# Kernel optimization log

Measured on AMD Instinct MI355X. Metric: run time of the kernel, lower is better.

The kernel has to match this reference:

```python
import jax, jax.numpy as jnp
import numpy as np

N, E, H, C = 50000, 800000, 4, 32   # nodes, edges, heads, per-head channels
EMB = 64                              # embedding_dim
VOCAB = 1000                          # input_dim (label vocab)


def _gat_layer(x, src, dst, W, a_src, a_dst, b):
    """PyG GATConv (concat heads, negative_slope=0.2, self-loops already in src/dst)."""
    n = x.shape[0]
    h = (x @ W).reshape(n, H, -1)                 # [N,H,C]
    al_s = (h * a_src).sum(-1)                    # [N,H]
    al_d = (h * a_dst).sum(-1)                    # [N,H]
    e = jax.nn.leaky_relu(al_s[src] + al_d[dst], 0.2)   # [E',H]
    m = jax.ops.segment_max(e, dst, num_segments=n)     # segment softmax (stable)
    p = jnp.exp(e - m[dst])
    s = jax.ops.segment_sum(p, dst, num_segments=n)
    alpha = p / (s[dst] + 1e-16)                  # [E',H]
    out = jax.ops.segment_sum(h[src] * alpha[..., None], dst, num_segments=n)
    return out.reshape(n, -1) + b                 # [N,H*C]


def setup_inputs() -> dict:
    key = jax.random.key(0)
    ks = jax.random.split(key, 16)
    def w(k, shape):
        return jax.random.normal(k, shape, jnp.float32) * 0.1
    return dict(
        label=jax.random.randint(ks[0], (N,), 0, VOCAB),
        edge_index=jax.random.randint(ks[1], (2, E), 0, N),
        weight=jax.random.uniform(ks[2], (E,), jnp.float32),
        request_quantity=jax.random.uniform(ks[3], (N,), jnp.float32),
        emb_table=w(ks[4], (VOCAB, EMB)),
        req_W=w(ks[5], (1, EMB)),
        req_b=jnp.zeros((EMB,), jnp.float32),
        W0=w(ks[6], (2 * EMB, H * C)), a_src0=w(ks[7], (H, C)), a_dst0=w(ks[8], (H, C)), b0=jnp.zeros((H * C,), jnp.float32),
        W1=w(ks[9], (H * C, H * C)), a_src1=w(ks[10], (H, C)), a_dst1=w(ks[11], (H, C)), b1=jnp.zeros((H * C,), jnp.float32),
        W2=w(ks[12], (H * C, H * C)), a_src2=w(ks[13], (H, C)), a_dst2=w(ks[14], (H, C)), b2=jnp.zeros((H * C,), jnp.float32),
    )


def reference(label, edge_index, weight, request_quantity, emb_table, req_W, req_b,
              W0, a_src0, a_dst0, b0, W1, a_src1, a_dst1, b1, W2, a_src2, a_dst2, b2):
    del weight  # GATConv(edge_dim=None): edge weights are not used in attention
    x_emb = emb_table[label]                                  # [N,EMB]
    rq = request_quantity
    rq = (rq - rq.mean()) / (rq.std(ddof=1) + 1e-6)           # torch std uses ddof=1
    req = rq[:, None] @ req_W + req_b                         # [N,EMB]
    x = jnp.concatenate([x_emb, req], axis=-1)                # [N,2*EMB]
    # PyG GATConv adds self-loops by default
    loops = jnp.arange(N)
    src = jnp.concatenate([edge_index[0], loops])
    dst = jnp.concatenate([edge_index[1], loops])
    gelu = lambda t: jax.nn.gelu(t, approximate=False)        # torch nn.GELU is exact
    x = gelu(_gat_layer(x, src, dst, W0, a_src0, a_dst0, b0))
    x = gelu(_gat_layer(x, src, dst, W1, a_src1, a_dst1, b1))
    x = gelu(_gat_layer(x, src, dst, W2, a_src2, a_dst2, b2))
    return x
```

## Files before the change

### kernel.cpp

```cpp
#include <hip/hip_runtime.h>
#include <hip/hip_fp16.h>
#include <math.h>

#define NN 50000
#define NE 800000
#define HC 128
#define NHEAD 4
#define EMB 64
#define STATS_BLOCKS 64
#define NB 196
#define HIST_BLOCKS 196
#define WPREP_BLOCKS 192
#define WT_ROW 136

typedef _Float16 f16x8 __attribute__((ext_vector_type(8)));
typedef float f32x4 __attribute__((ext_vector_type(4)));

__device__ __forceinline__ float lrelu(float x) { return x > 0.0f ? x : 0.2f * x; }
__device__ __forceinline__ float gelu_f(float x) {
    return 0.5f * x * (1.0f + erff(x * 0.70710678118654752440f));
}
__device__ __forceinline__ float sel4(float4 v, int h) {
    float r = v.x;
    r = (h == 1) ? v.y : r;
    r = (h == 2) ? v.z : r;
    r = (h == 3) ? v.w : r;
    return r;
}
__device__ __forceinline__ f16x8 cvt8(float4 a, float4 b) {
    f16x8 v;
    v[0] = (_Float16)a.x; v[1] = (_Float16)a.y; v[2] = (_Float16)a.z; v[3] = (_Float16)a.w;
    v[4] = (_Float16)b.x; v[5] = (_Float16)b.y; v[6] = (_Float16)b.z; v[7] = (_Float16)b.w;
    return v;
}

__global__ void prep_kernel(const float* __restrict__ rq, float* __restrict__ stats,
                            const int* __restrict__ dst, int* __restrict__ bucketCnt,
                            const float* __restrict__ W0, const float* __restrict__ W1,
                            const float* __restrict__ W2, _Float16* __restrict__ wt) {
    __shared__ float ls[4], ls2[4];
    __shared__ int cnt[NB];
    if (blockIdx.x < STATS_BLOCKS) {
        int i = blockIdx.x * 256 + threadIdx.x;
        float s = 0.f, s2 = 0.f;
        for (; i < NN; i += STATS_BLOCKS * 256) {
            float v = rq[i];
            s += v; s2 += v * v;
        }
        #pragma unroll
        for (int off = 32; off > 0; off >>= 1) {
            s  += __shfl_down(s, off);
            s2 += __shfl_down(s2, off);
        }
        int lane = threadIdx.x & 63, wid = threadIdx.x >> 6;
        if (lane == 0) { ls[wid] = s; ls2[wid] = s2; }
        __syncthreads();
        if (threadIdx.x == 0) {
            atomicAdd(&stats[0], ls[0] + ls[1] + ls[2] + ls[3]);
            atomicAdd(&stats[1], ls2[0] + ls2[1] + ls2[2] + ls2[3]);
        }
    } else if (blockIdx.x < STATS_BLOCKS + HIST_BLOCKS) {
        int bb = blockIdx.x - STATS_BLOCKS;
        for (int i = threadIdx.x; i < NB; i += 256) cnt[i] = 0;
        __syncthreads();
        int base = bb * 4096;
        #pragma unroll
        for (int it = 0; it < 16; it++) {
            int i = base + it * 256 + threadIdx.x;
            if (i < NE) atomicAdd(&cnt[dst[i] >> 8], 1);
        }
        __syncthreads();
        for (int i = threadIdx.x; i < NB; i += 256)
            if (cnt[i]) atomicAdd(&bucketCnt[i], cnt[i]);
    } else {
        int bb = blockIdx.x - STATS_BLOCKS - HIST_BLOCKS;
        int l = bb >> 6, blk = bb & 63;
        const float* W = (l == 0) ? W0 : (l == 1) ? W1 : W2;
        int idx = blk * 256 + threadIdx.x;
        int n = idx >> 7, k = idx & 127;
        wt[(size_t)l * 128 * WT_ROW + n * WT_ROW + k] = (_Float16)W[k * 128 + n];
    }
}

__device__ __forceinline__ void scan_buckets(const int* __restrict__ bucketCnt,
                                             int* sIncl ) {
    int t = threadIdx.x;
    int v = (t < NB) ? bucketCnt[t] : 0;
    sIncl[t] = v;
    __syncthreads();
    #pragma unroll
    for (int off = 1; off < 256; off <<= 1) {
        int add = (t >= off) ? sIncl[t - off] : 0;
        __syncthreads();
        sIncl[t] += add;
        __syncthreads();
    }
}

__global__ void binA_kernel(const int* __restrict__ src, const int* __restrict__ dst,
                            const int* __restrict__ bucketCnt, int* __restrict__ gcur,
                            int2* __restrict__ edge_tmp) {
    __shared__ int sIncl[256];
    __shared__ int sBaseE[256];
    __shared__ int cnt[NB];
    __shared__ int cur[NB];
    int t = threadIdx.x;
    scan_buckets(bucketCnt, sIncl);
    {
        int v = (t < NB) ? bucketCnt[t] : 0;
        sBaseE[t] = sIncl[t] - v;
    }
    for (int i = t; i < NB; i += 256) cnt[i] = 0;
    __syncthreads();
    int base = blockIdx.x * 4096;
    int d[16], s[16];
    #pragma unroll
    for (int it = 0; it < 16; it++) {
        int i = base + it * 256 + t;
        bool ok = i < NE;
        d[it] = ok ? dst[i] : -1;
        s[it] = ok ? src[i] : 0;
        if (ok) atomicAdd(&cnt[d[it] >> 8], 1);
    }
    __syncthreads();
    for (int i = t; i < NB; i += 256)
        cur[i] = cnt[i] ? (sBaseE[i] + atomicAdd(&gcur[i], cnt[i])) : 0;
    __syncthreads();
    #pragma unroll
    for (int it = 0; it < 16; it++) {
        if (d[it] >= 0) {
            int b = d[it] >> 8;
            int pos = atomicAdd(&cur[b], 1);
            edge_tmp[pos] = make_int2(s[it], d[it] & 255);
        }
    }
}

__global__ void binB_kernel(const int2* __restrict__ edge_tmp, const int* __restrict__ bucketCnt,
                            int* __restrict__ row_start, int* __restrict__ src_sorted) {
    __shared__ int sIncl[256];
    __shared__ int ldeg[256];
    __shared__ int lexcl[256];
    __shared__ int lcur[256];
    __shared__ int s_base, s_end;
    int b = blockIdx.x, t = threadIdx.x;
    scan_buckets(bucketCnt, sIncl);
    if (t == 0) {
        s_end = sIncl[b];
        s_base = sIncl[b] - bucketCnt[b];
    }
    ldeg[t] = 0;
    __syncthreads();
    int base = s_base, endb = s_end;
    for (int i = base + t; i < endb; i += 256)
        atomicAdd(&ldeg[edge_tmp[i].y], 1);
    __syncthreads();
    int v = ldeg[t];
    lexcl[t] = v;
    __syncthreads();
    #pragma unroll
    for (int off = 1; off < 256; off <<= 1) {
        int add = (t >= off) ? lexcl[t - off] : 0;
        __syncthreads();
        lexcl[t] += add;
        __syncthreads();
    }
    int excl = lexcl[t] - v;
    int node = b * 256 + t;
    if (node <= NN) row_start[node] = base + excl;
    lcur[t] = excl;
    __syncthreads();
    for (int i = base + t; i < endb; i += 256) {
        int2 e = edge_tmp[i];
        int pos = atomicAdd(&lcur[e.y], 1);
        src_sorted[base + pos] = e.x;
    }
}

template <int L0>
__launch_bounds__(256)
__global__ void gemm_al_kernel(const __half* __restrict__ xh, const _Float16* __restrict__ wt,
                               const float* __restrict__ a_src, const float* __restrict__ a_dst,
                               __half* __restrict__ h, float* __restrict__ als,
                               float* __restrict__ ald,
                               const int* __restrict__ label, const float* __restrict__ rq,
                               const float* __restrict__ emb, const float* __restrict__ reqW,
                               const float* __restrict__ reqb, const float* __restrict__ stats) {
    extern __shared__ char smem[];
    _Float16* sWt = (_Float16*)smem;
    _Float16* sX  = sWt + 128 * WT_ROW;
    int t = threadIdx.x;
    int w = t >> 6, l = t & 63;
    int col = l & 15, quad = l >> 4;
    int row0 = blockIdx.x * 64;

    {
        const f16x8* g = (const f16x8*)wt;
        f16x8* s = (f16x8*)sWt;
        #pragma unroll
        for (int i = 0; i < 9; i++) {
            int idx = t + 256 * i;
            if (idx < 128 * WT_ROW / 8) s[idx] = g[idx];
        }
    }
    if (L0) {
        float sum = stats[0], sumsq = stats[1];
        float mean = sum / (float)NN;
        float var = (sumsq - sum * sum / (float)NN) / (float)(NN - 1);
        float inv = 1.0f / (sqrtf(var) + 1e-6f);
        #pragma unroll
        for (int i = 0; i < 4; i++) {
            int idx = t + 256 * i;
            int r = idx >> 4;
            int q = idx & 15;
            int rr = row0 + r;
            f16x8 v;
            #pragma unroll
            for (int j = 0; j < 8; j++) v[j] = (_Float16)0.f;
            if (rr < NN) {
                if (q < 8) {
                    const float4* er = (const float4*)(emb + (size_t)label[rr] * EMB);
                    v = cvt8(er[q * 2], er[q * 2 + 1]);
                } else {
                    int j4 = (q - 8) * 2;
                    float4 w0 = ((const float4*)reqW)[j4],     b0 = ((const float4*)reqb)[j4];
                    float4 w1 = ((const float4*)reqW)[j4 + 1], b1 = ((const float4*)reqb)[j4 + 1];
                    float r2 = (rq[rr] - mean) * inv;
                    v = cvt8(make_float4(r2 * w0.x + b0.x, r2 * w0.y + b0.y,
                                         r2 * w0.z + b0.z, r2 * w0.w + b0.w),
                             make_float4(r2 * w1.x + b1.x, r2 * w1.y + b1.y,
                                         r2 * w1.z + b1.z, r2 * w1.w + b1.w));
                }
            }
            *(f16x8*)&sX[r * WT_ROW + q * 8] = v;
        }
    }
    __syncthreads();

    f16x8 afr[4];
    if (L0) {
        #pragma unroll
        for (int ks = 0; ks < 4; ks++)
            afr[ks] = *(const f16x8*)&sX[(w * 16 + col) * WT_ROW + ks * 32 + quad * 8];
    } else {
        int rr = row0 + w * 16 + col;
        const __half* xp = xh + (size_t)rr * 128;
        #pragma unroll
        for (int ks = 0; ks < 4; ks++)
            afr[ks] = *(const f16x8*)(xp + ks * 32 + quad * 8);
    }

    f32x4 zero = {0.f, 0.f, 0.f, 0.f};
    f32x4 acc[8];
    #pragma unroll
    for (int nt = 0; nt < 8; nt++) acc[nt] = zero;
    #pragma unroll
    for (int nt = 0; nt < 8; nt++) {
        #pragma unroll
        for (int ks = 0; ks < 4; ks++) {
            f16x8 bfr = *(const f16x8*)&sWt[(nt * 16 + col) * WT_ROW + ks * 32 + quad * 8];
            acc[nt] = __builtin_amdgcn_mfma_f32_16x16x32_f16(afr[ks], bfr, acc[nt], 0, 0, 0);
        }
    }
    __syncthreads();

    _Float16* sOut = sWt;
    #pragma unroll
    for (int nt = 0; nt < 8; nt++)
        #pragma unroll
        for (int r = 0; r < 4; r++)
            sOut[(w * 16 + quad * 4 + r) * WT_ROW + nt * 16 + col] = (_Float16)acc[nt][r];
    __builtin_amdgcn_wave_barrier();
    #pragma unroll
    for (int i = 0; i < 4; i++) {
        int u = l + 64 * i;
        int r = u >> 4, off = (u & 15) * 8;
        int rr = row0 + w * 16 + r;
        f16x8 v = *(const f16x8*)&sOut[(w * 16 + r) * WT_ROW + off];
        if (rr < NN) *(f16x8*)(h + (size_t)rr * 128 + off) = v;
    }

    float as[8], ad[8];
    #pragma unroll
    for (int nt = 0; nt < 8; nt++) {
        as[nt] = a_src[nt * 16 + col];
        ad[nt] = a_dst[nt * 16 + col];
    }
    #pragma unroll
    for (int r = 0; r < 4; r++) {
        float ps[4], pd[4];
        #pragma unroll
        for (int hd = 0; hd < 4; hd++) {
            ps[hd] = acc[2 * hd][r] * as[2 * hd] + acc[2 * hd + 1][r] * as[2 * hd + 1];
            pd[hd] = acc[2 * hd][r] * ad[2 * hd] + acc[2 * hd + 1][r] * ad[2 * hd + 1];
            ps[hd] += __shfl_xor(ps[hd], 1); pd[hd] += __shfl_xor(pd[hd], 1);
            ps[hd] += __shfl_xor(ps[hd], 2); pd[hd] += __shfl_xor(pd[hd], 2);
            ps[hd] += __shfl_xor(ps[hd], 4); pd[hd] += __shfl_xor(pd[hd], 4);
            ps[hd] += __shfl_xor(ps[hd], 8); pd[hd] += __shfl_xor(pd[hd], 8);
        }
        int rr = row0 + w * 16 + quad * 4 + r;
        if (col == 0 && rr < NN) {
            *(float4*)(als + (size_t)rr * 4) = make_float4(ps[0], ps[1], ps[2], ps[3]);
            *(float4*)(ald + (size_t)rr * 4) = make_float4(pd[0], pd[1], pd[2], pd[3]);
        }
    }
}

template <int FINAL>
__launch_bounds__(256)
__global__ void agg_kernel(const __half* __restrict__ h, const float* __restrict__ als_,
                           const float* __restrict__ ald_, const int* __restrict__ row_start,
                           const int* __restrict__ src_sorted, const float* __restrict__ bias,
                           float* __restrict__ outf, __half* __restrict__ outh) {
    __shared__ float lds_p[4][4][68];
    __shared__ int   lds_s[4][64];
    int wid = threadIdx.x >> 6;
    int lane = threadIdx.x & 63;
    int node = blockIdx.x * 4 + wid;
    if (node >= NN) return;
    int sub  = lane >> 4;
    int cg   = lane & 15;
    int c0   = cg * 8;
    int head = cg >> 2;

    int start = row_start[node], end = row_start[node + 1];
    float4 adv = *(const float4*)(ald_ + (size_t)node * 4);
    float4 avs = *(const float4*)(als_ + (size_t)node * 4);

    float p_self = __expf(lrelu(sel4(avs, head) + sel4(adv, head)));
    float pinit = (sub == 0) ? p_self : 0.f;
    float s_sum = pinit;
    float acc[8];
    {
        float4 raw = *(const float4*)(h + (size_t)node * 128 + c0);
        const __half2* q2 = (const __half2*)&raw;
        #pragma unroll
        for (int i = 0; i < 4; i++) {
            float2 f = __half22float2(q2[i]);
            acc[2 * i] = f.x * pinit;
            acc[2 * i + 1] = f.y * pinit;
        }
    }

    for (int base = start; base < end; base += 64) {
        int j = base + lane;
        int my = 0;
        float4 p4 = make_float4(0.f, 0.f, 0.f, 0.f);
        if (j < end) {
            my = src_sorted[j];
            float4 av = *(const float4*)(als_ + (size_t)my * 4);
            p4.x = __expf(lrelu(av.x + adv.x));
            p4.y = __expf(lrelu(av.y + adv.y));
            p4.z = __expf(lrelu(av.z + adv.z));
            p4.w = __expf(lrelu(av.w + adv.w));
        }
        lds_s[wid][lane] = my;
        lds_p[wid][0][lane] = p4.x;
        lds_p[wid][1][lane] = p4.y;
        lds_p[wid][2][lane] = p4.z;
        lds_p[wid][3][lane] = p4.w;
        __builtin_amdgcn_wave_barrier();

        int cnt = end - base;
        if (cnt > 64) cnt = 64;
        for (int jj = 0; jj < cnt; jj += 16) {
            int   s[4];
            float p[4];
            #pragma unroll
            for (int i = 0; i < 4; i++) {
                int e = jj + 4 * i + sub;
                bool v = e < cnt;
                int ec = v ? e : 0;
                s[i] = lds_s[wid][ec];
                float pv = lds_p[wid][head][ec];
                p[i] = v ? pv : 0.f;
            }
            float4 raw[4];
            #pragma unroll
            for (int i = 0; i < 4; i++)
                raw[i] = *(const float4*)(h + (size_t)s[i] * 128 + c0);
            #pragma unroll
            for (int i = 0; i < 4; i++) {
                const __half2* q2 = (const __half2*)&raw[i];
                float2 f0 = __half22float2(q2[0]);
                float2 f1 = __half22float2(q2[1]);
                float2 f2 = __half22float2(q2[2]);
                float2 f3 = __half22float2(q2[3]);
                s_sum += p[i];
                acc[0] += f0.x * p[i]; acc[1] += f0.y * p[i];
                acc[2] += f1.x * p[i]; acc[3] += f1.y * p[i];
                acc[4] += f2.x * p[i]; acc[5] += f2.y * p[i];
                acc[6] += f3.x * p[i]; acc[7] += f3.y * p[i];
            }
        }
        __builtin_amdgcn_wave_barrier();
    }

    #pragma unroll
    for (int i = 0; i < 8; i++) {
        acc[i] += __shfl_xor(acc[i], 16);
        acc[i] += __shfl_xor(acc[i], 32);
    }
    s_sum += __shfl_xor(s_sum, 16);
    s_sum += __shfl_xor(s_sum, 32);

    float invs = 1.0f / (s_sum + 1e-16f);
    float t0 = (sub & 1) ? acc[2] : acc[0];
    float t1 = (sub & 1) ? acc[6] : acc[4];
    float num0 = (sub & 2) ? t1 : t0;
    float u0 = (sub & 1) ? acc[3] : acc[1];
    float u1 = (sub & 1) ? acc[7] : acc[5];
    float num1 = (sub & 2) ? u1 : u0;
    int cc = c0 + 2 * sub;
    float2 bv = *(const float2*)(bias + cc);
    float o0 = gelu_f(num0 * invs + bv.x);
    float o1 = gelu_f(num1 * invs + bv.y);
    if (FINAL) {
        *(float2*)(outf + (size_t)node * 128 + cc) = make_float2(o0, o1);
    } else {
        *(__half2*)(outh + (size_t)node * 128 + cc) = __floats2half2_rn(o0, o1);
    }
}

extern "C" void kernel_launch(void* const* d_in, const int* in_sizes, int n_in,
                              void* d_out, int out_size, void* d_ws, size_t ws_size,
                              hipStream_t stream) {
    const int*   label = (const int*)d_in[0];
    const int*   eidx  = (const int*)d_in[1];
    const float* rq    = (const float*)d_in[3];
    const float* emb   = (const float*)d_in[4];
    const float* reqW  = (const float*)d_in[5];
    const float* reqb  = (const float*)d_in[6];
    const float* W[3]    = {(const float*)d_in[7],  (const float*)d_in[11], (const float*)d_in[15]};
    const float* asrc[3] = {(const float*)d_in[8],  (const float*)d_in[12], (const float*)d_in[16]};
    const float* adst[3] = {(const float*)d_in[9],  (const float*)d_in[13], (const float*)d_in[17]};
    const float* bias[3] = {(const float*)d_in[10], (const float*)d_in[14], (const float*)d_in[18]};

    const int* e_src = eidx;
    const int* e_dst = eidx + NE;

    char* ws = (char*)d_ws;
    size_t off = 0;
    auto A = [&](size_t n) { size_t o = off; off += (n + 255) & ~(size_t)255; return o; };
    size_t o_bcnt  = A(256 * 4);
    size_t o_gcur  = A(256 * 4);
    size_t o_stats = A(8);
    size_t zero_bytes = off;
    size_t o_row   = A((size_t)(NN + 1) * 4);
    size_t o_etmp  = A((size_t)NE * 8);
    size_t o_srcS  = A((size_t)NE * 4);
    size_t o_wt    = A((size_t)3 * 128 * WT_ROW * 2);
    size_t o_x     = A((size_t)NN * 128 * 2);
    size_t o_h     = A((size_t)NN * 128 * 2);
    size_t o_als   = A((size_t)NN * 4 * 4);
    size_t o_ald   = A((size_t)NN * 4 * 4);
    (void)ws_size; (void)n_in; (void)in_sizes; (void)out_size;

    int*      bcnt  = (int*)(ws + o_bcnt);
    int*      gcur  = (int*)(ws + o_gcur);
    float*    stats = (float*)(ws + o_stats);
    int*      rowst = (int*)(ws + o_row);
    int2*     etmp  = (int2*)(ws + o_etmp);
    int*      srcS  = (int*)(ws + o_srcS);
    _Float16* wt    = (_Float16*)(ws + o_wt);
    __half*   xh    = (__half*)(ws + o_x);
    __half*   h     = (__half*)(ws + o_h);
    float*    als   = (float*)(ws + o_als);
    float*    ald   = (float*)(ws + o_ald);

    (void)hipMemsetAsync(ws, 0, zero_bytes, stream);

    prep_kernel<<<STATS_BLOCKS + HIST_BLOCKS + WPREP_BLOCKS, 256, 0, stream>>>(
        rq, stats, e_dst, bcnt, W[0], W[1], W[2], wt);
    binA_kernel<<<HIST_BLOCKS, 256, 0, stream>>>(e_src, e_dst, bcnt, gcur, etmp);
    binB_kernel<<<NB, 256, 0, stream>>>(etmp, bcnt, rowst, srcS);

    const int gemm_blocks = (NN + 63) / 64;
    const int agg_blocks = (NN + 3) / 4;
    const int smem_l0 = (128 + 64) * WT_ROW * 2;
    const int smem_ln = 128 * WT_ROW * 2;
    for (int l = 0; l < 3; l++) {
        const _Float16* wtl = wt + (size_t)l * 128 * WT_ROW;
        if (l == 0)
            gemm_al_kernel<1><<<gemm_blocks, 256, smem_l0, stream>>>(
                xh, wtl, asrc[l], adst[l], h, als, ald, label, rq, emb, reqW, reqb, stats);
        else
            gemm_al_kernel<0><<<gemm_blocks, 256, smem_ln, stream>>>(
                xh, wtl, asrc[l], adst[l], h, als, ald, label, rq, emb, reqW, reqb, stats);
        if (l == 2)
            agg_kernel<1><<<agg_blocks, 256, 0, stream>>>(h, als, ald, rowst, srcS, bias[l],
                                                          (float*)d_out, nullptr);
        else
            agg_kernel<0><<<agg_blocks, 256, 0, stream>>>(h, als, ald, rowst, srcS, bias[l],
                                                          nullptr, xh);
    }
}
```

Baseline: 293.3 us.

## Assign four destination nodes per wave in GAT aggregation, one per quarter-wave

The aggregation kernel now maps four consecutive destination nodes to each wave, with each 16-lane group owning one node, instead of one node per wave split across four edge subsets. Edge indices and attention weights for the wave's combined contiguous CSR range are staged together in LDS as int2 pairs, and each lane takes its node's destination logits through shuffles. This removes the cross-group shuffle reduction and the masked partial iterations left over when a node's degree is small. The cost is load imbalance between the four groups when degrees differ, since groups sit idle while the longest node finishes. The output is now written as 8-wide vector stores.

```diff
diff --git a/kernel.cpp b/kernel.cpp
--- a/kernel.cpp
+++ b/kernel.cpp
@@ -312,113 +312,96 @@
                            const float* __restrict__ ald_, const int* __restrict__ row_start,
                            const int* __restrict__ src_sorted, const float* __restrict__ bias,
                            float* __restrict__ outf, __half* __restrict__ outh) {
-    __shared__ float lds_p[4][4][68];
-    __shared__ int   lds_s[4][64];
-    int wid = threadIdx.x >> 6;
+    __shared__ int2 lds_sp[4][4][66];
+    int wid  = threadIdx.x >> 6;
     int lane = threadIdx.x & 63;
-    int node = blockIdx.x * 4 + wid;
-    if (node >= NN) return;
-    int sub  = lane >> 4;
+    int g    = lane >> 4;
     int cg   = lane & 15;
     int c0   = cg * 8;
     int head = cg >> 2;
 
-    int start = row_start[node], end = row_start[node + 1];
+    int nb = blockIdx.x * 16 + wid * 4;
+    if (nb >= NN) return;
+    int node = nb + g;
+
+    int rs = row_start[node];
+    int re = row_start[node + 1];
+    int start = __shfl(rs, 0);
+    int end   = __shfl(re, 48);
+    int b1 = __shfl(rs, 16), b2 = __shfl(rs, 32), b3 = __shfl(rs, 48);
+
     float4 adv = *(const float4*)(ald_ + (size_t)node * 4);
     float4 avs = *(const float4*)(als_ + (size_t)node * 4);
 
     float p_self = __expf(lrelu(sel4(avs, head) + sel4(adv, head)));
-    float pinit = (sub == 0) ? p_self : 0.f;
-    float s_sum = pinit;
+    float s_sum = p_self;
     float acc[8];
     {
-        float4 raw = *(const float4*)(h + (size_t)node * 128 + c0);
-        const __half2* q2 = (const __half2*)&raw;
-        #pragma unroll
-        for (int i = 0; i < 4; i++) {
-            float2 f = __half22float2(q2[i]);
-            acc[2 * i] = f.x * pinit;
-            acc[2 * i + 1] = f.y * pinit;
-        }
+        f16x8 hv = *(const f16x8*)(h + (size_t)node * 128 + c0);
+        #pragma unroll
+        for (int j = 0; j < 8; j++) acc[j] = (float)hv[j] * p_self;
     }
 
     for (int base = start; base < end; base += 64) {
         int j = base + lane;
-        int my = 0;
-        float4 p4 = make_float4(0.f, 0.f, 0.f, 0.f);
-        if (j < end) {
-            my = src_sorted[j];
-            float4 av = *(const float4*)(als_ + (size_t)my * 4);
-            p4.x = __expf(lrelu(av.x + adv.x));
-            p4.y = __expf(lrelu(av.y + adv.y));
-            p4.z = __expf(lrelu(av.z + adv.z));
-            p4.w = __expf(lrelu(av.w + adv.w));
-        }
-        lds_s[wid][lane] = my;
-        lds_p[wid][0][lane] = p4.x;
-        lds_p[wid][1][lane] = p4.y;
-        lds_p[wid][2][lane] = p4.z;
-        lds_p[wid][3][lane] = p4.w;
+        bool v = j < end;
+        int my = v ? src_sorted[j] : 0;
+        float4 av = *(const float4*)(als_ + (size_t)my * 4);
+        int o = (j >= b1) + (j >= b2) + (j >= b3);
+        int ol = o << 4;
+        float dx = __shfl(adv.x, ol), dy = __shfl(adv.y, ol);
+        float dz = __shfl(adv.z, ol), dw = __shfl(adv.w, ol);
+        lds_sp[wid][0][lane] = make_int2(my, __float_as_int(__expf(lrelu(av.x + dx))));
+        lds_sp[wid][1][lane] = make_int2(my, __float_as_int(__expf(lrelu(av.y + dy))));
+        lds_sp[wid][2][lane] = make_int2(my, __float_as_int(__expf(lrelu(av.z + dz))));
+        lds_sp[wid][3][lane] = make_int2(my, __float_as_int(__expf(lrelu(av.w + dw))));
         __builtin_amdgcn_wave_barrier();
 
-        int cnt = end - base;
-        if (cnt > 64) cnt = 64;
-        for (int jj = 0; jj < cnt; jj += 16) {
-            int   s[4];
-            float p[4];
+        int lo  = rs > base ? rs : base;
+        int hiw = base + 64;
+        int hi  = re < hiw ? re : hiw;
+        for (int k = lo; k < hi; k += 4) {
+            int sidx[4]; float p[4];
             #pragma unroll
             for (int i = 0; i < 4; i++) {
-                int e = jj + 4 * i + sub;
-                bool v = e < cnt;
-                int ec = v ? e : 0;
-                s[i] = lds_s[wid][ec];
-                float pv = lds_p[wid][head][ec];
-                p[i] = v ? pv : 0.f;
+                int e = k + i;
+                bool val = e < hi;
+                int ec = (val ? e : hi - 1) - base;
+                int2 sp = lds_sp[wid][head][ec];
+                sidx[i] = sp.x;
+                p[i] = val ? __int_as_float(sp.y) : 0.f;
             }
-            float4 raw[4];
+            f16x8 raw[4];
             #pragma unroll
             for (int i = 0; i < 4; i++)
-                raw[i] = *(const float4*)(h + (size_t)s[i] * 128 + c0);
+                raw[i] = *(const f16x8*)(h + (size_t)sidx[i] * 128 + c0);
             #pragma unroll
             for (int i = 0; i < 4; i++) {
-                const __half2* q2 = (const __half2*)&raw[i];
-                float2 f0 = __half22float2(q2[0]);
-                float2 f1 = __half22float2(q2[1]);
-                float2 f2 = __half22float2(q2[2]);
-                float2 f3 = __half22float2(q2[3]);
                 s_sum += p[i];
-                acc[0] += f0.x * p[i]; acc[1] += f0.y * p[i];
-                acc[2] += f1.x * p[i]; acc[3] += f1.y * p[i];
-                acc[4] += f2.x * p[i]; acc[5] += f2.y * p[i];
-                acc[6] += f3.x * p[i]; acc[7] += f3.y * p[i];
+                #pragma unroll
+                for (int jj = 0; jj < 8; jj++)
+                    acc[jj] += (float)raw[i][jj] * p[i];
             }
         }
         __builtin_amdgcn_wave_barrier();
     }
 
-    #pragma unroll
-    for (int i = 0; i < 8; i++) {
-        acc[i] += __shfl_xor(acc[i], 16);
-        acc[i] += __shfl_xor(acc[i], 32);
-    }
-    s_sum += __shfl_xor(s_sum, 16);
-    s_sum += __shfl_xor(s_sum, 32);
-
     float invs = 1.0f / (s_sum + 1e-16f);
-    float t0 = (sub & 1) ? acc[2] : acc[0];
-    float t1 = (sub & 1) ? acc[6] : acc[4];
-    float num0 = (sub & 2) ? t1 : t0;
-    float u0 = (sub & 1) ? acc[3] : acc[1];
-    float u1 = (sub & 1) ? acc[7] : acc[5];
-    float num1 = (sub & 2) ? u1 : u0;
-    int cc = c0 + 2 * sub;
-    float2 bv = *(const float2*)(bias + cc);
-    float o0 = gelu_f(num0 * invs + bv.x);
-    float o1 = gelu_f(num1 * invs + bv.y);
+    float4 bv0 = *(const float4*)(bias + c0);
+    float4 bv1 = *(const float4*)(bias + c0 + 4);
+    float ob[8] = {bv0.x, bv0.y, bv0.z, bv0.w, bv1.x, bv1.y, bv1.z, bv1.w};
+    float o8[8];
+    #pragma unroll
+    for (int jj = 0; jj < 8; jj++) o8[jj] = gelu_f(acc[jj] * invs + ob[jj]);
     if (FINAL) {
-        *(float2*)(outf + (size_t)node * 128 + cc) = make_float2(o0, o1);
+        float* op = outf + (size_t)node * 128 + c0;
+        *(float4*)op       = make_float4(o8[0], o8[1], o8[2], o8[3]);
+        *(float4*)(op + 4) = make_float4(o8[4], o8[5], o8[6], o8[7]);
     } else {
-        *(__half2*)(outh + (size_t)node * 128 + cc) = __floats2half2_rn(o0, o1);
+        f16x8 hv;
+        #pragma unroll
+        for (int jj = 0; jj < 8; jj++) hv[jj] = (_Float16)o8[jj];
+        *(f16x8*)(outh + (size_t)node * 128 + c0) = hv;
     }
 }
 
@@ -476,7 +459,7 @@
     binB_kernel<<<NB, 256, 0, stream>>>(etmp, bcnt, rowst, srcS);
 
     const int gemm_blocks = (NN + 63) / 64;
-    const int agg_blocks = (NN + 3) / 4;
+    const int agg_blocks = (NN + 15) / 16;
     const int smem_l0 = (128 + 64) * WT_ROW * 2;
     const int smem_ln = 128 * WT_ROW * 2;
     for (int l = 0; l < 3; l++) {
```

Result: no change. 296.7 us (+1.2%).
